# Performance work log

Measured on AMD Instinct MI355X. Metric: run time of the kernel, lower is better.

## Reference

```python
import jax, jax.numpy as jnp
import numpy as np
import math

D_MODEL = 1024
N_HEADS = 16
HEAD_DIM = D_MODEL // N_HEADS
MLP_DIM = 4 * D_MODEL
B, L, M = 2, 2048, 2048


def layer_norm(x, g, b, eps=1e-5):
    mu = jnp.mean(x, axis=-1, keepdims=True)
    var = jnp.var(x, axis=-1, keepdims=True)
    return (x - mu) * jax.lax.rsqrt(var + eps) * g + b


def mha(q_in, k_in, qW, wW, oW, mask=None):
    # Faithful to source: k and v share w_proj, and the value einsum uses k.
    b, l, _ = q_in.shape
    m = k_in.shape[1]
    q = (q_in @ qW).reshape(b, l, HEAD_DIM, N_HEADS)
    k = (k_in @ wW).reshape(b, m, HEAD_DIM, N_HEADS)
    s = jnp.einsum('bldn,bmdn->blmn', q, k)
    if mask is not None:
        s = jnp.where(mask, -1e9, s)  # mask applied BEFORE scaling, as in source
    s = s / math.sqrt(HEAD_DIM)
    w = jax.nn.softmax(s, axis=2)
    x = jnp.einsum('blmn,bmdn->bldn', w, k)  # source bug: uses k, not v
    x = x.reshape(b, l, HEAD_DIM * N_HEADS)
    return x @ oW


def setup_inputs() -> dict:
    key = jax.random.key(0)
    ks = jax.random.split(key, 16)
    sc = 1.0 / math.sqrt(D_MODEL)
    inp = {
        'x': jax.random.normal(ks[0], (B, L, D_MODEL), jnp.float32),
        'enc_output': jax.random.normal(ks[1], (B, M, D_MODEL), jnp.float32),
        'mask': jax.random.randint(ks[2], (B, 1, M, 1), 0, 2).astype(bool),
        'q1W': jax.random.normal(ks[3], (D_MODEL, D_MODEL), jnp.float32) * sc,
        'w1W': jax.random.normal(ks[4], (D_MODEL, D_MODEL), jnp.float32) * sc,
        'o1W': jax.random.normal(ks[5], (D_MODEL, D_MODEL), jnp.float32) * sc,
        'q2W': jax.random.normal(ks[6], (D_MODEL, D_MODEL), jnp.float32) * sc,
        'w2W': jax.random.normal(ks[7], (D_MODEL, D_MODEL), jnp.float32) * sc,
        'o2W': jax.random.normal(ks[8], (D_MODEL, D_MODEL), jnp.float32) * sc,
        'ffW1': jax.random.normal(ks[9], (D_MODEL, MLP_DIM), jnp.float32) * sc,
        'ffb1': jnp.zeros((MLP_DIM,), jnp.float32),
        'ffW2': jax.random.normal(ks[10], (MLP_DIM, D_MODEL), jnp.float32) * sc,
        'ffb2': jnp.zeros((D_MODEL,), jnp.float32),
        'g1': jnp.ones((D_MODEL,), jnp.float32), 'b1': jnp.zeros((D_MODEL,), jnp.float32),
        'g2': jnp.ones((D_MODEL,), jnp.float32), 'b2': jnp.zeros((D_MODEL,), jnp.float32),
        'g3': jnp.ones((D_MODEL,), jnp.float32), 'b3': jnp.zeros((D_MODEL,), jnp.float32),
    }
    return inp


def reference(x, enc_output, mask, q1W, w1W, o1W, q2W, w2W, o2W,
              ffW1, ffb1, ffW2, ffb2, g1, b1, g2, b2, g3, b3):
    # self-attention (no mask, as in source)
    sa = mha(x, x, q1W, w1W, o1W, mask=None)
    x = layer_norm(x + sa, g1, b1)
    # encoder-decoder attention with mask
    ca = mha(x, enc_output, q2W, w2W, o2W, mask=mask)
    x = layer_norm(x + ca, g2, b2)
    # feed-forward (exact GELU, matching torch nn.GELU default)
    h = jax.nn.gelu(x @ ffW1 + ffb1, approximate=False)
    ff = h @ ffW2 + ffb2
    x = layer_norm(x + ff, g3, b3)
    return x
```

## Files before the change

kernel.cpp:

```cpp
#include <hip/hip_runtime.h>
#include <hip/hip_bf16.h>
#include <math.h>
#include <stdint.h>

typedef __attribute__((ext_vector_type(8))) short bf16x8_t;
typedef __attribute__((ext_vector_type(4))) float f32x4_t;

#define LOG2E 1.4426950408889634f
#define GLB(p) ((const __attribute__((address_space(1))) void*)(p))
#define LDS(p) ((__attribute__((address_space(3))) void*)(p))

__device__ __forceinline__ unsigned short f2bf(float f) {
    union { float f; unsigned int u; } v; v.f = f;
    unsigned int r = v.u + 0x7FFFu + ((v.u >> 16) & 1u);
    return (unsigned short)(r >> 16);
}

__device__ __forceinline__ float bf2f(unsigned short us) {
    union { unsigned int u; float f; } c; c.u = (unsigned int)us << 16; return c.f;
}

__device__ __forceinline__ unsigned int pack2bf(float a, float b) {
#if __has_builtin(__builtin_amdgcn_cvt_pk_bf16_f32)
    auto r = __builtin_amdgcn_cvt_pk_bf16_f32(a, b);
    unsigned int u;
    __builtin_memcpy(&u, &r, 4);
    return u;
#else
    return (unsigned int)f2bf(a) | ((unsigned int)f2bf(b) << 16);
#endif
}

__device__ __forceinline__ float fast_rcp(float x) {
#if __has_builtin(__builtin_amdgcn_rcpf)
    return __builtin_amdgcn_rcpf(x);
#else
    return 1.0f / x;
#endif
}

__device__ __forceinline__ float gelu_fast(float v) {
    float x2 = v * v;
    float inner = v * fmaf(0.0356774081f, x2, 0.7978845608f);
    inner = fminf(fmaxf(inner, -20.f), 20.f);
    float t = exp2f(inner * 2.8853900817779268f);
    return v * t * fast_rcp(t + 1.0f);
}

__global__ void cast2_bf16_k(const float* __restrict__ inA, unsigned short* __restrict__ outA,
                             const float* __restrict__ inB, unsigned short* __restrict__ outB,
                             int n4, const int* __restrict__ maskp, float* __restrict__ mask4) {
    if (blockIdx.y == 2) {
        int i = blockIdx.x * blockDim.x + threadIdx.x;
        if (i < 8192) {
            int nt = i & 3, l16 = (i >> 2) & 15, t = (i >> 6) & 31, b = (i >> 11) & 1;
            mask4[i] = maskp[b * 2048 + t * 64 + nt * 16 + l16] ? -1e10f : 0.0f;
        }
        return;
    }
    const float* in = blockIdx.y ? inB : inA;
    unsigned short* out = blockIdx.y ? outB : outA;
    int i = blockIdx.x * blockDim.x + threadIdx.x;
    if (i < n4) {
        float4 v = ((const float4*)in)[i];
        ushort4 o;
        o.x = f2bf(v.x); o.y = f2bf(v.y); o.z = f2bf(v.z); o.w = f2bf(v.w);
        ((ushort4*)out)[i] = o;
    }
}

__global__ void transpose_all_k(const float* __restrict__ s0, const float* __restrict__ s1,
                                const float* __restrict__ s2, const float* __restrict__ s3,
                                const float* __restrict__ s4, const float* __restrict__ s5,
                                const float* __restrict__ s6, const float* __restrict__ s7,
                                unsigned short* __restrict__ d0, unsigned short* __restrict__ d1,
                                unsigned short* __restrict__ d2, unsigned short* __restrict__ d3,
                                unsigned short* __restrict__ d4, unsigned short* __restrict__ d5,
                                unsigned short* __restrict__ d6, unsigned short* __restrict__ d7) {
    __shared__ float tile[32][33];
    int idx = blockIdx.x;
    const float* W; unsigned short* Wt; int K, N, bx, by;
    if (idx < 6144) {
        int which = idx >> 10, t = idx & 1023;
        bx = t & 31; by = t >> 5; K = 1024; N = 1024;
        switch (which) {
            case 0: W = s0; Wt = d0; break;
            case 1: W = s1; Wt = d1; break;
            case 2: W = s2; Wt = d2; break;
            case 3: W = s3; Wt = d3; break;
            case 4: W = s4; Wt = d4; break;
            default: W = s5; Wt = d5; break;
        }
    } else if (idx < 10240) {
        int t = idx - 6144;
        bx = t & 127; by = t >> 7; K = 1024; N = 4096;
        W = s6; Wt = d6;
    } else {
        int t = idx - 10240;
        bx = t & 31; by = t >> 5; K = 4096; N = 1024;
        W = s7; Wt = d7;
    }
    int k0 = by * 32, n0 = bx * 32;
    int tx = threadIdx.x, ty = threadIdx.y;
#pragma unroll
    for (int i = 0; i < 32; i += 8)
        tile[ty + i][tx] = W[(long)(k0 + ty + i) * N + n0 + tx];
    __syncthreads();
#pragma unroll
    for (int i = 0; i < 32; i += 8)
        Wt[(long)(n0 + ty + i) * K + k0 + tx] = f2bf(tile[tx][ty + i]);
}

__global__ __launch_bounds__(256) void split_qk_k(const unsigned short* __restrict__ inQ,
                                                  const unsigned short* __restrict__ inK,
                                                  int stride, int koff,
                                                  unsigned short* __restrict__ Qout,
                                                  unsigned short* __restrict__ Kout) {
    __shared__ __align__(16) unsigned short t[16][1024];
    long l0 = (long)blockIdx.x * 16;
    int tid = threadIdx.x;
    int h = tid >> 4, lr = tid & 15;
    long l = l0 + lr;
    int b = (int)(l >> 11);
    int ll = (int)(l & 2047);
    int sw = ll & 7;

    for (int c = tid; c < 2048; c += 256) {
        int r = c >> 7, col = (c & 127) * 8;
        *(uint4*)(&t[r][col]) = *(const uint4*)(inQ + (l0 + r) * stride + col);
    }
    __syncthreads();
    {
        unsigned short* op = Qout + ((long)(b * 16 + h) * 2048 + ll) * 64;
#pragma unroll
        for (int g = 0; g < 8; g++) {
            union { uint4 v; unsigned short s[8]; } u;
#pragma unroll
            for (int j = 0; j < 8; j++) u.s[j] = t[lr][(g * 8 + j) * 16 + h];
            *(uint4*)(op + (g ^ sw) * 8) = u.v;
        }
    }
    __syncthreads();
    for (int c = tid; c < 2048; c += 256) {
        int r = c >> 7, col = (c & 127) * 8;
        *(uint4*)(&t[r][col]) = *(const uint4*)(inK + (l0 + r) * stride + koff + col);
    }
    __syncthreads();
    {
        unsigned short* op = Kout + ((long)(b * 16 + h) * 2048 + ll) * 64;
#pragma unroll
        for (int g = 0; g < 8; g++) {
            union { uint4 v; unsigned short s[8]; } u;
#pragma unroll
            for (int j = 0; j < 8; j++) u.s[j] = t[lr][(g * 8 + j) * 16 + h];
            *(uint4*)(op + (g ^ sw) * 8) = u.v;
        }
    }
}

__global__ __launch_bounds__(256) void transpose_heads_perm_k(const unsigned short* __restrict__ in,
                                                              unsigned short* __restrict__ out) {
    __shared__ unsigned short t[64][72];
    int bh = blockIdx.y;
    int m0 = blockIdx.x * 64;
    int tid = threadIdx.x;
    for (int c = tid; c < 512; c += 256) {
        int r = c >> 3, gp = c & 7;
        int glog = gp ^ (r & 7);
        uint4 v = *(const uint4*)(in + ((long)bh * 2048 + m0 + r) * 64 + gp * 8);
        *(uint4*)(&t[r][glog * 8]) = v;
    }
    __syncthreads();
    for (int c = tid; c < 512; c += 256) {
        int d = c >> 3, pb = (c & 7) * 8;
        union { uint4 v; unsigned short s[8]; } u;
#pragma unroll
        for (int j = 0; j < 8; j++) {
            int p = pb + j;
            int m = (p >> 2) + (p & 3) * 16;
            u.s[j] = t[m][d];
        }
        int gph = (pb >> 3) ^ (d & 7);
        *(uint4*)(out + ((long)bh * 64 + d) * 2048 + m0 + gph * 8) = u.v;
    }
}

template <int EP, int BN>
__global__ __launch_bounds__(256) void gemm_k(const unsigned short* __restrict__ A,
                                              const unsigned short* __restrict__ Bt,
                                              void* __restrict__ outp,
                                              const float* __restrict__ bias,
                                              int M, int N, int K) {
    __shared__ __align__(16) unsigned short As[128 * 64];
    __shared__ __align__(16) unsigned short Bs[BN * 64];
    const int NT = BN / 32;
    const int BG = BN / 32;
    int tid = threadIdx.x;
    int wave = tid >> 6, lane = tid & 63;
    int wm = wave >> 1, wn = wave & 1;
    int quad = lane >> 4, l16 = lane & 15;
    int bm = blockIdx.y * 128, bn = blockIdx.x * BN;

    f32x4_t acc[4][NT] = {};

    int srow = tid >> 3;
    int sgrp = (tid & 7) ^ (srow & 7);
    const unsigned short* Ag[4];
#pragma unroll
    for (int i = 0; i < 4; i++)
        Ag[i] = A + (long)(bm + i * 32 + srow) * K + sgrp * 8;
    const unsigned short* Bg[BG];
#pragma unroll
    for (int i = 0; i < BG; i++)
        Bg[i] = Bt + (long)(bn + i * 32 + srow) * K + sgrp * 8;

    for (int k0 = 0; k0 < K; k0 += 64) {
        __syncthreads();
#pragma unroll
        for (int i = 0; i < 4; i++)
            __builtin_amdgcn_global_load_lds(GLB(Ag[i] + k0), LDS(As + i * 2048 + tid * 8), 16, 0, 0);
#pragma unroll
        for (int i = 0; i < BG; i++)
            __builtin_amdgcn_global_load_lds(GLB(Bg[i] + k0), LDS(Bs + i * 2048 + tid * 8), 16, 0, 0);
        __syncthreads();
#pragma unroll
        for (int kk = 0; kk < 2; kk++) {
            int xg = ((kk * 4 + quad) ^ (l16 & 7)) * 8;
            bf16x8_t af[4], bfr[NT];
#pragma unroll
            for (int t = 0; t < 4; t++)
                af[t] = *(const bf16x8_t*)(As + (wm * 64 + t * 16 + l16) * 64 + xg);
#pragma unroll
            for (int t = 0; t < NT; t++)
                bfr[t] = *(const bf16x8_t*)(Bs + (wn * (BN / 2) + t * 16 + l16) * 64 + xg);
#pragma unroll
            for (int mt = 0; mt < 4; mt++)
#pragma unroll
                for (int nt = 0; nt < NT; nt++)
                    acc[mt][nt] = __builtin_amdgcn_mfma_f32_16x16x32_bf16(af[mt], bfr[nt], acc[mt][nt], 0, 0, 0);
        }
    }

#pragma unroll
    for (int mt = 0; mt < 4; mt++)
#pragma unroll
        for (int nt = 0; nt < NT; nt++)
#pragma unroll
            for (int r = 0; r < 4; r++) {
                int gm = bm + wm * 64 + mt * 16 + quad * 4 + r;
                int gn = bn + wn * (BN / 2) + nt * 16 + l16;
                float v = acc[mt][nt][r];
                if (EP == 0) {
                    ((float*)outp)[(long)gm * N + gn] = v;
                } else if (EP == 2) {
                    v = gelu_fast(v + bias[gn]);
                    ((unsigned short*)outp)[(long)gm * N + gn] = f2bf(v);
                } else if (EP == 3) {
                    ((float*)outp)[(long)gm * N + gn] = v + bias[gn];
                } else if (EP == 6) {
                    ((unsigned short*)outp)[(long)gm * N + gn] = f2bf(v + bias[gn]);
                } else {
                    ((unsigned short*)outp)[(long)gm * N + gn] = f2bf(v);
                }
            }
}

template <int EP>
__global__ __launch_bounds__(512, 4) void gemm8_k(const unsigned short* __restrict__ A,
                                                  const unsigned short* __restrict__ Bt,
                                                  void* __restrict__ outp,
                                                  const float* __restrict__ bias,
                                                  const unsigned short* __restrict__ A2,
                                                  const unsigned short* __restrict__ Bt2,
                                                  void* __restrict__ out2,
                                                  int M, int N, int K) {
    if (blockIdx.z) { A = A2; Bt = Bt2; outp = out2; }
    __shared__ __align__(16) unsigned short As[2 * 128 * 64];
    __shared__ __align__(16) unsigned short Bs[2 * 128 * 64];
    int tid = threadIdx.x;
    int wave = tid >> 6, lane = tid & 63;
    int wm = wave >> 2, wn = wave & 3;
    int quad = lane >> 4, l16 = lane & 15;
    int bm = blockIdx.y * 128, bn = blockIdx.x * 128;

    f32x4_t acc[4][2] = {};

    int srow = tid >> 3;
    int sgrp = (tid & 7) ^ (srow & 7);
    const unsigned short* Ag[2];
    const unsigned short* Bg[2];
#pragma unroll
    for (int i = 0; i < 2; i++) {
        Ag[i] = A + (long)(bm + i * 64 + srow) * K + sgrp * 8;
        Bg[i] = Bt + (long)(bn + i * 64 + srow) * K + sgrp * 8;
    }

    auto stage = [&](int buf, int k0) {
#pragma unroll
        for (int i = 0; i < 2; i++)
            __builtin_amdgcn_global_load_lds(GLB(Ag[i] + k0), LDS(As + buf * 8192 + i * 4096 + tid * 8), 16, 0, 0);
#pragma unroll
        for (int i = 0; i < 2; i++)
            __builtin_amdgcn_global_load_lds(GLB(Bg[i] + k0), LDS(Bs + buf * 8192 + i * 4096 + tid * 8), 16, 0, 0);
    };

    auto compute = [&](int buf) {
        const unsigned short* Ab = As + buf * 8192;
        const unsigned short* Bb = Bs + buf * 8192;
#pragma unroll
        for (int kk = 0; kk < 2; kk++) {
            int xg = ((kk * 4 + quad) ^ (l16 & 7)) * 8;
            bf16x8_t af[4], bfr[2];
#pragma unroll
            for (int t = 0; t < 4; t++)
                af[t] = *(const bf16x8_t*)(Ab + (wm * 64 + t * 16 + l16) * 64 + xg);
#pragma unroll
            for (int t = 0; t < 2; t++)
                bfr[t] = *(const bf16x8_t*)(Bb + (wn * 32 + t * 16 + l16) * 64 + xg);
#pragma unroll
            for (int mt = 0; mt < 4; mt++)
#pragma unroll
                for (int nt = 0; nt < 2; nt++)
                    acc[mt][nt] = __builtin_amdgcn_mfma_f32_16x16x32_bf16(af[mt], bfr[nt], acc[mt][nt], 0, 0, 0);
        }
    };

    stage(0, 0);
    const int NS = K >> 6;
    for (int i = 0; i < NS; i++) {
        if (i + 1 < NS) {
            stage((i + 1) & 1, (i + 1) << 6);
            asm volatile("s_waitcnt vmcnt(4)\n\ts_barrier" ::: "memory");
        } else {
            asm volatile("s_waitcnt vmcnt(0)\n\ts_barrier" ::: "memory");
        }
        compute(i & 1);
        asm volatile("s_barrier" ::: "memory");
    }

#pragma unroll
    for (int mt = 0; mt < 4; mt++)
#pragma unroll
        for (int nt = 0; nt < 2; nt++)
#pragma unroll
            for (int r = 0; r < 4; r++) {
                int gm = bm + wm * 64 + mt * 16 + quad * 4 + r;
                int gn = bn + wn * 32 + nt * 16 + l16;
                float v = acc[mt][nt][r];
                if (EP == 6) {
                    ((unsigned short*)outp)[(long)gm * N + gn] = f2bf(v + bias[gn]);
                } else {
                    ((unsigned short*)outp)[(long)gm * N + gn] = f2bf(v);
                }
            }
}

template <int USE_MASK>
__global__ __launch_bounds__(256, 4) void flash_attn9_k(const unsigned short* __restrict__ Qh,
                                                        const unsigned short* __restrict__ Kh,
                                                        const unsigned short* __restrict__ KhTp,
                                                        const float* __restrict__ mask4,
                                                        unsigned short* __restrict__ out) {
    __shared__ __align__(16) unsigned short K1[64 * 64];
    __shared__ __align__(16) unsigned short K2[64 * 64];
    __shared__ __align__(16) unsigned short Ps[64 * 64];
    __shared__ __align__(16) float Ml[USE_MASK ? 2048 : 4];

    int tid = threadIdx.x;
    int wave = tid >> 6, lane = tid & 63;
    int quad = lane >> 4, l16 = lane & 15;
    int bh = blockIdx.y, b = bh >> 4, h = bh & 15;
    int l0 = blockIdx.x * 64;
    const unsigned short* k1p = Kh + (long)bh * 2048 * 64 + tid * 8;
    const unsigned short* k2p = KhTp + (long)bh * 64 * 2048 + (long)(tid >> 3) * 2048 + (tid & 7) * 8;

    int sw = l16 & 7;

    const unsigned short* qrow = Qh + ((long)bh * 2048 + l0 + wave * 16 + l16) * 64;
    bf16x8_t qf[2];
#pragma unroll
    for (int kk = 0; kk < 2; kk++)
        qf[kk] = *(const bf16x8_t*)(qrow + ((kk * 4 + quad) ^ sw) * 8);

    __builtin_amdgcn_global_load_lds(GLB(k1p), LDS(K1 + tid * 8), 16, 0, 0);
    __builtin_amdgcn_global_load_lds(GLB(k1p + 2048), LDS(K1 + tid * 8 + 2048), 16, 0, 0);
    __builtin_amdgcn_global_load_lds(GLB(k2p), LDS(K2 + tid * 8), 16, 0, 0);
    __builtin_amdgcn_global_load_lds(GLB(k2p + 32 * 2048), LDS(K2 + tid * 8 + 2048), 16, 0, 0);
    if (USE_MASK) {
        const float* mp = mask4 + b * 2048;
        for (int c = tid; c < 512; c += 256)
            ((float4*)Ml)[c] = ((const float4*)mp)[c];
    }
    __syncthreads();

    const float C1 = 0.125f * LOG2E;
    f32x4_t acc_o[4] = {};
    float rs[4] = {0.f, 0.f, 0.f, 0.f};

    for (int t = 0; t < 32; ++t) {
        uint4 rA, rB, rC, rD;
        if (t < 31) {
            k1p += 4096;
            k2p += 64;
            rA = *(const uint4*)(k1p);
            rB = *(const uint4*)(k1p + 2048);
            rC = *(const uint4*)(k2p);
            rD = *(const uint4*)(k2p + 32 * 2048);
        }

        float4 mq = make_float4(0.f, 0.f, 0.f, 0.f);
        if (USE_MASK) mq = *(const float4*)(Ml + t * 64 + l16 * 4);

        f32x4_t sacc[4] = {};
        __builtin_amdgcn_s_setprio(1);
#pragma unroll
        for (int kk = 0; kk < 2; kk++) {
            int xg = ((kk * 4 + quad) ^ sw) * 8;
#pragma unroll
            for (int nt = 0; nt < 4; nt++) {
                bf16x8_t bfr = *(const bf16x8_t*)(K1 + (nt * 16 + l16) * 64 + xg);
                sacc[nt] = __builtin_amdgcn_mfma_f32_16x16x32_bf16(qf[kk], bfr, sacc[nt], 0, 0, 0);
            }
        }
        __builtin_amdgcn_s_setprio(0);

#pragma unroll
        for (int r = 0; r < 4; r++) {
            float p0 = exp2f(fmaf(sacc[0][r], C1, mq.x));
            float p1 = exp2f(fmaf(sacc[1][r], C1, mq.y));
            float p2 = exp2f(fmaf(sacc[2][r], C1, mq.z));
            float p3 = exp2f(fmaf(sacc[3][r], C1, mq.w));
            rs[r] += (p0 + p1) + (p2 + p3);
            uint2 pk; pk.x = pack2bf(p0, p1); pk.y = pack2bf(p2, p3);
            int Rrow = wave * 16 + quad * 4 + r;
            int grp = (l16 >> 1) ^ (Rrow & 7);
            *(uint2*)(Ps + Rrow * 64 + grp * 8 + (l16 & 1) * 4) = pk;
        }

        __builtin_amdgcn_s_setprio(1);
#pragma unroll
        for (int kk = 0; kk < 2; kk++) {
            int xg = ((kk * 4 + quad) ^ sw) * 8;
            int Rr = wave * 16 + l16;
            int pg = ((kk * 4 + quad) ^ (l16 & 7)) * 8;
            bf16x8_t af = *(const bf16x8_t*)(Ps + Rr * 64 + pg);
#pragma unroll
            for (int nt = 0; nt < 4; nt++) {
                bf16x8_t bfr = *(const bf16x8_t*)(K2 + (nt * 16 + l16) * 64 + xg);
                acc_o[nt] = __builtin_amdgcn_mfma_f32_16x16x32_bf16(af, bfr, acc_o[nt], 0, 0, 0);
            }
        }
        __builtin_amdgcn_s_setprio(0);

        asm volatile("s_barrier" ::: "memory");
        if (t < 31) {
            *(uint4*)(K1 + tid * 8) = rA;
            *(uint4*)(K1 + tid * 8 + 2048) = rB;
            *(uint4*)(K2 + tid * 8) = rC;
            *(uint4*)(K2 + tid * 8 + 2048) = rD;
            asm volatile("s_waitcnt lgkmcnt(0)\n\ts_barrier" ::: "memory");
        }
    }

#pragma unroll
    for (int r = 0; r < 4; r++) {
#pragma unroll
        for (int d = 1; d < 16; d <<= 1) rs[r] += __shfl_xor(rs[r], d);
    }

#pragma unroll
    for (int r = 0; r < 4; r++) {
        float inv = 1.0f / rs[r];
        int l = l0 + wave * 16 + quad * 4 + r;
#pragma unroll
        for (int nt = 0; nt < 4; nt++) {
            int d = nt * 16 + l16;
            out[((long)(b * 2048 + l)) * 1024 + d * 16 + h] = f2bf(acc_o[nt][r] * inv);
        }
    }
}

template <int AIN_BF16, int OUT_F32>
__global__ __launch_bounds__(256) void resid_ln_k(const void* __restrict__ ap,
                                                  const unsigned short* __restrict__ rb,
                                                  const float* __restrict__ g,
                                                  const float* __restrict__ bb,
                                                  float* __restrict__ outf,
                                                  unsigned short* __restrict__ outb) {
    long row = blockIdx.x;
    int tid = threadIdx.x;
    float x0, x1, x2, x3;
    if (AIN_BF16) {
        ushort4 va = ((const ushort4*)((const unsigned short*)ap + row * 1024))[tid];
        x0 = bf2f(va.x); x1 = bf2f(va.y); x2 = bf2f(va.z); x3 = bf2f(va.w);
    } else {
        float4 va = ((const float4*)((const float*)ap + row * 1024))[tid];
        x0 = va.x; x1 = va.y; x2 = va.z; x3 = va.w;
    }
    ushort4 vr = ((const ushort4*)(rb + row * 1024))[tid];
    x0 += bf2f(vr.x); x1 += bf2f(vr.y); x2 += bf2f(vr.z); x3 += bf2f(vr.w);
    float s = x0 + x1 + x2 + x3;
    float sq = x0 * x0 + x1 * x1 + x2 * x2 + x3 * x3;
#pragma unroll
    for (int d = 1; d < 64; d <<= 1) { s += __shfl_xor(s, d); sq += __shfl_xor(sq, d); }
    __shared__ float ss[4], ssq[4];
    int wave = tid >> 6, lane = tid & 63;
    if (lane == 0) { ss[wave] = s; ssq[wave] = sq; }
    __syncthreads();
    s = ss[0] + ss[1] + ss[2] + ss[3];
    sq = ssq[0] + ssq[1] + ssq[2] + ssq[3];
    float mean = s * (1.0f / 1024.0f);
    float var = sq * (1.0f / 1024.0f) - mean * mean;
    float rstd = rsqrtf(var + 1e-5f);
    float4 vg = ((const float4*)g)[tid];
    float4 vb = ((const float4*)bb)[tid];
    float y0 = (x0 - mean) * rstd * vg.x + vb.x;
    float y1 = (x1 - mean) * rstd * vg.y + vb.y;
    float y2 = (x2 - mean) * rstd * vg.z + vb.z;
    float y3 = (x3 - mean) * rstd * vg.w + vb.w;
    if (OUT_F32) {
        float4 o; o.x = y0; o.y = y1; o.z = y2; o.w = y3;
        ((float4*)(outf + row * 1024))[tid] = o;
    } else {
        ushort4 ob; ob.x = f2bf(y0); ob.y = f2bf(y1); ob.z = f2bf(y2); ob.w = f2bf(y3);
        ((ushort4*)(outb + row * 1024))[tid] = ob;
    }
}

extern "C" void kernel_launch(void* const* d_in, const int* in_sizes, int n_in,
                              void* d_out, int out_size, void* d_ws, size_t ws_size,
                              hipStream_t stream) {
    const float* x    = (const float*)d_in[0];
    const float* enc  = (const float*)d_in[1];
    const int*   mask = (const int*)d_in[2];
    const float* q1W  = (const float*)d_in[3];
    const float* w1W  = (const float*)d_in[4];
    const float* o1W  = (const float*)d_in[5];
    const float* q2W  = (const float*)d_in[6];
    const float* w2W  = (const float*)d_in[7];
    const float* o2W  = (const float*)d_in[8];
    const float* ffW1 = (const float*)d_in[9];
    const float* ffb1 = (const float*)d_in[10];
    const float* ffW2 = (const float*)d_in[11];
    const float* ffb2 = (const float*)d_in[12];
    const float* g1 = (const float*)d_in[13];
    const float* b1 = (const float*)d_in[14];
    const float* g2 = (const float*)d_in[15];
    const float* b2 = (const float*)d_in[16];
    const float* g3 = (const float*)d_in[17];
    const float* b3 = (const float*)d_in[18];
    float* outp = (float*)d_out;

    const int T = 4096;
    const int D = 1024;
    const int F = 4096;

    char* ws = (char*)d_ws;
    auto alloc = [&](size_t sz) { char* p = ws; ws += (sz + 255) & ~(size_t)255; return p; };
    unsigned short* qw1Wt = (unsigned short*)alloc((size_t)2 * D * D * 2);
    unsigned short* o1Wt  = (unsigned short*)alloc((size_t)D * D * 2);
    unsigned short* q2Wt  = (unsigned short*)alloc((size_t)D * D * 2);
    unsigned short* w2Wt  = (unsigned short*)alloc((size_t)D * D * 2);
    unsigned short* o2Wt  = (unsigned short*)alloc((size_t)D * D * 2);
    unsigned short* ffW1t = (unsigned short*)alloc((size_t)F * D * 2);
    unsigned short* ffW2t = (unsigned short*)alloc((size_t)D * F * 2);
    unsigned short* xb    = (unsigned short*)alloc((size_t)T * D * 2);
    unsigned short* encb  = (unsigned short*)alloc((size_t)T * D * 2);
    unsigned short* Qhb   = (unsigned short*)alloc((size_t)T * D * 2);
    unsigned short* Khb   = (unsigned short*)alloc((size_t)T * D * 2);
    unsigned short* KhTb  = (unsigned short*)alloc((size_t)T * D * 2);
    unsigned short* attnb = (unsigned short*)alloc((size_t)T * D * 2);
    float*          mask4b= (float*)alloc((size_t)8192 * 4);
    unsigned short* projb = (unsigned short*)alloc((size_t)T * D * 2);
    unsigned short* x1s   = (unsigned short*)alloc((size_t)T * D * 2);
    unsigned short* x2s   = (unsigned short*)alloc((size_t)T * D * 2);
    unsigned short* S1    = (unsigned short*)alloc((size_t)T * F * 2);
    unsigned short* tmpqw = S1;
    unsigned short* q2o   = S1;
    unsigned short* w2o   = S1 + (size_t)T * D;
    unsigned short* hb    = S1;

    dim3 blk256(256);
    dim3 blk512(512);
    dim3 tblk(32, 8);

    cast2_bf16_k<<<dim3(T * D / 4 / 256, 3), blk256, 0, stream>>>(x, xb, enc, encb, T * D / 4, mask, mask4b);
    transpose_all_k<<<dim3(14336), tblk, 0, stream>>>(
        q1W, w1W, o1W, q2W, w2W, o2W, ffW1, ffW2,
        qw1Wt, qw1Wt + (size_t)D * D, o1Wt, q2Wt, w2Wt, o2Wt, ffW1t, ffW2t);

    gemm8_k<4><<<dim3(2 * D / 128, T / 128, 1), blk512, 0, stream>>>(
        xb, qw1Wt, tmpqw, nullptr, nullptr, nullptr, nullptr, T, 2 * D, D);
    split_qk_k<<<dim3(T / 16), blk256, 0, stream>>>(tmpqw, tmpqw, 2 * D, D, Qhb, Khb);
    transpose_heads_perm_k<<<dim3(32, 32), blk256, 0, stream>>>(Khb, KhTb);
    flash_attn9_k<0><<<dim3(32, 32), blk256, 0, stream>>>(Qhb, Khb, KhTb, nullptr, attnb);
    gemm8_k<4><<<dim3(D / 128, T / 128, 1), blk512, 0, stream>>>(
        attnb, o1Wt, projb, nullptr, nullptr, nullptr, nullptr, T, D, D);
    resid_ln_k<0, 0><<<dim3(T), blk256, 0, stream>>>(x, projb, g1, b1, nullptr, x1s);

    gemm8_k<4><<<dim3(D / 128, T / 128, 2), blk512, 0, stream>>>(
        x1s, q2Wt, q2o, nullptr, encb, w2Wt, w2o, T, D, D);
    split_qk_k<<<dim3(T / 16), blk256, 0, stream>>>(q2o, w2o, D, 0, Qhb, Khb);
    transpose_heads_perm_k<<<dim3(32, 32), blk256, 0, stream>>>(Khb, KhTb);
    flash_attn9_k<1><<<dim3(32, 32), blk256, 0, stream>>>(Qhb, Khb, KhTb, mask4b, attnb);
    gemm8_k<4><<<dim3(D / 128, T / 128, 1), blk512, 0, stream>>>(
        attnb, o2Wt, projb, nullptr, nullptr, nullptr, nullptr, T, D, D);
    resid_ln_k<1, 0><<<dim3(T), blk256, 0, stream>>>(x1s, projb, g2, b2, nullptr, x2s);

    gemm_k<2, 128><<<dim3(F / 128, T / 128, 1), blk256, 0, stream>>>(
        x2s, ffW1t, hb, ffb1, T, F, D);
    gemm8_k<6><<<dim3(D / 128, T / 128, 1), blk512, 0, stream>>>(
        hb, ffW2t, projb, ffb2, nullptr, nullptr, nullptr, T, D, F);
    resid_ln_k<1, 1><<<dim3(T), blk256, 0, stream>>>(x2s, projb, g3, b3, outp, nullptr);
}
```

Before: 560.8 us.

## Fuse head split and K transpose into Q/K projection GEMM epilogue

The Q/K projection GEMMs now stage their bf16 output tile in shared memory and write Q, K and the permuted transposed K straight into head-major swizzled layouts. This removes the separate split_qk and transpose_heads kernels along with the round trip through an intermediate buffer. Exp2 calls in the attention softmax and GELU are also switched to the hardware exp2 intrinsic. In exchange, the GEMM epilogue gains extra LDS traffic, a block-wide sync and less coalesced scattered stores.

```diff
diff --git a/kernel.cpp b/kernel.cpp
--- a/kernel.cpp
+++ b/kernel.cpp
@@ -39,11 +39,19 @@
 #endif
 }
 
+__device__ __forceinline__ float fexp2(float x) {
+#if __has_builtin(__builtin_amdgcn_exp2f)
+    return __builtin_amdgcn_exp2f(x);
+#else
+    return exp2f(x);
+#endif
+}
+
 __device__ __forceinline__ float gelu_fast(float v) {
     float x2 = v * v;
     float inner = v * fmaf(0.0356774081f, x2, 0.7978845608f);
     inner = fminf(fmaxf(inner, -20.f), 20.f);
-    float t = exp2f(inner * 2.8853900817779268f);
+    float t = fexp2(inner * 2.8853900817779268f);
     return v * t * fast_rcp(t + 1.0f);
 }
 
@@ -111,80 +119,6 @@
         Wt[(long)(n0 + ty + i) * K + k0 + tx] = f2bf(tile[tx][ty + i]);
 }
 
-__global__ __launch_bounds__(256) void split_qk_k(const unsigned short* __restrict__ inQ,
-                                                  const unsigned short* __restrict__ inK,
-                                                  int stride, int koff,
-                                                  unsigned short* __restrict__ Qout,
-                                                  unsigned short* __restrict__ Kout) {
-    __shared__ __align__(16) unsigned short t[16][1024];
-    long l0 = (long)blockIdx.x * 16;
-    int tid = threadIdx.x;
-    int h = tid >> 4, lr = tid & 15;
-    long l = l0 + lr;
-    int b = (int)(l >> 11);
-    int ll = (int)(l & 2047);
-    int sw = ll & 7;
-
-    for (int c = tid; c < 2048; c += 256) {
-        int r = c >> 7, col = (c & 127) * 8;
-        *(uint4*)(&t[r][col]) = *(const uint4*)(inQ + (l0 + r) * stride + col);
-    }
-    __syncthreads();
-    {
-        unsigned short* op = Qout + ((long)(b * 16 + h) * 2048 + ll) * 64;
-#pragma unroll
-        for (int g = 0; g < 8; g++) {
-            union { uint4 v; unsigned short s[8]; } u;
-#pragma unroll
-            for (int j = 0; j < 8; j++) u.s[j] = t[lr][(g * 8 + j) * 16 + h];
-            *(uint4*)(op + (g ^ sw) * 8) = u.v;
-        }
-    }
-    __syncthreads();
-    for (int c = tid; c < 2048; c += 256) {
-        int r = c >> 7, col = (c & 127) * 8;
-        *(uint4*)(&t[r][col]) = *(const uint4*)(inK + (l0 + r) * stride + koff + col);
-    }
-    __syncthreads();
-    {
-        unsigned short* op = Kout + ((long)(b * 16 + h) * 2048 + ll) * 64;
-#pragma unroll
-        for (int g = 0; g < 8; g++) {
-            union { uint4 v; unsigned short s[8]; } u;
-#pragma unroll
-            for (int j = 0; j < 8; j++) u.s[j] = t[lr][(g * 8 + j) * 16 + h];
-            *(uint4*)(op + (g ^ sw) * 8) = u.v;
-        }
-    }
-}
-
-__global__ __launch_bounds__(256) void transpose_heads_perm_k(const unsigned short* __restrict__ in,
-                                                              unsigned short* __restrict__ out) {
-    __shared__ unsigned short t[64][72];
-    int bh = blockIdx.y;
-    int m0 = blockIdx.x * 64;
-    int tid = threadIdx.x;
-    for (int c = tid; c < 512; c += 256) {
-        int r = c >> 3, gp = c & 7;
-        int glog = gp ^ (r & 7);
-        uint4 v = *(const uint4*)(in + ((long)bh * 2048 + m0 + r) * 64 + gp * 8);
-        *(uint4*)(&t[r][glog * 8]) = v;
-    }
-    __syncthreads();
-    for (int c = tid; c < 512; c += 256) {
-        int d = c >> 3, pb = (c & 7) * 8;
-        union { uint4 v; unsigned short s[8]; } u;
-#pragma unroll
-        for (int j = 0; j < 8; j++) {
-            int p = pb + j;
-            int m = (p >> 2) + (p & 3) * 16;
-            u.s[j] = t[m][d];
-        }
-        int gph = (pb >> 3) ^ (d & 7);
-        *(uint4*)(out + ((long)bh * 64 + d) * 2048 + m0 + gph * 8) = u.v;
-    }
-}
-
 template <int EP, int BN>
 __global__ __launch_bounds__(256) void gemm_k(const unsigned short* __restrict__ A,
                                               const unsigned short* __restrict__ Bt,
@@ -250,15 +184,9 @@
                 int gm = bm + wm * 64 + mt * 16 + quad * 4 + r;
                 int gn = bn + wn * (BN / 2) + nt * 16 + l16;
                 float v = acc[mt][nt][r];
-                if (EP == 0) {
-                    ((float*)outp)[(long)gm * N + gn] = v;
-                } else if (EP == 2) {
+                if (EP == 2) {
                     v = gelu_fast(v + bias[gn]);
                     ((unsigned short*)outp)[(long)gm * N + gn] = f2bf(v);
-                } else if (EP == 3) {
-                    ((float*)outp)[(long)gm * N + gn] = v + bias[gn];
-                } else if (EP == 6) {
-                    ((unsigned short*)outp)[(long)gm * N + gn] = f2bf(v + bias[gn]);
                 } else {
                     ((unsigned short*)outp)[(long)gm * N + gn] = f2bf(v);
                 }
@@ -272,11 +200,14 @@
                                                   const float* __restrict__ bias,
                                                   const unsigned short* __restrict__ A2,
                                                   const unsigned short* __restrict__ Bt2,
-                                                  void* __restrict__ out2,
+                                                  unsigned short* __restrict__ qout,
+                                                  unsigned short* __restrict__ kout,
+                                                  unsigned short* __restrict__ ktout,
                                                   int M, int N, int K) {
-    if (blockIdx.z) { A = A2; Bt = Bt2; outp = out2; }
-    __shared__ __align__(16) unsigned short As[2 * 128 * 64];
-    __shared__ __align__(16) unsigned short Bs[2 * 128 * 64];
+    if (blockIdx.z) { A = A2; Bt = Bt2; }
+    __shared__ __align__(16) unsigned short SMEM[32768];
+    unsigned short* As = SMEM;
+    unsigned short* Bs = SMEM + 16384;
     int tid = threadIdx.x;
     int wave = tid >> 6, lane = tid & 63;
     int wm = wave >> 2, wn = wave & 3;
@@ -336,6 +267,64 @@
         }
         compute(i & 1);
         asm volatile("s_barrier" ::: "memory");
+    }
+
+    if (EP == 7 || EP == 8) {
+        bool kmode = (EP == 7) ? (bn >= 1024) : (blockIdx.z != 0);
+        int G = (EP == 7 && kmode) ? ((bn - 1024) >> 7) : (bn >> 7);
+        unsigned short* Ct = SMEM;
+#pragma unroll
+        for (int mt = 0; mt < 4; mt++)
+#pragma unroll
+            for (int nt = 0; nt < 2; nt++)
+#pragma unroll
+                for (int r = 0; r < 4; r++) {
+                    int rr = wm * 64 + mt * 16 + quad * 4 + r;
+                    int cc = wn * 32 + nt * 16 + l16;
+                    Ct[rr * 132 + cc] = f2bf(acc[mt][nt][r]);
+                }
+        __syncthreads();
+        int bq = bm >> 11;
+        if (!kmode) {
+#pragma unroll
+            for (int i = 0; i < 4; i++) {
+                int e = tid + i * 512;
+                int h = e & 15, rl = e >> 4;
+                int ll = (bm & 2047) + rl;
+                union { uint4 v; unsigned short s[8]; } u;
+#pragma unroll
+                for (int j = 0; j < 8; j++) u.s[j] = Ct[rl * 132 + j * 16 + h];
+                *(uint4*)(qout + (((long)(bq * 16 + h) * 2048 + ll) << 6) + ((G ^ (ll & 7)) << 3)) = u.v;
+            }
+        } else {
+#pragma unroll
+            for (int i = 0; i < 4; i++) {
+                int e = tid + i * 512;
+                int h = e & 15, rl = e >> 4;
+                int mm = (bm & 2047) + rl;
+                union { uint4 v; unsigned short s[8]; } u;
+#pragma unroll
+                for (int j = 0; j < 8; j++) u.s[j] = Ct[rl * 132 + j * 16 + h];
+                *(uint4*)(kout + (((long)(bq * 16 + h) * 2048 + mm) << 6) + ((G ^ (mm & 7)) << 3)) = u.v;
+            }
+#pragma unroll
+            for (int i = 0; i < 4; i++) {
+                int e = tid + i * 512;
+                int glog = e & 7, m0s = (e >> 3) & 1, dl = (e >> 4) & 7, h = e >> 7;
+                int d = G * 8 + dl;
+                union { uint4 v; unsigned short s[8]; } u;
+#pragma unroll
+                for (int j = 0; j < 8; j++) {
+                    int p = glog * 8 + j;
+                    int ml = (p >> 2) + (p & 3) * 16;
+                    u.s[j] = Ct[(m0s * 64 + ml) * 132 + dl * 16 + h];
+                }
+                int mmbase = (bm & 2047) + m0s * 64;
+                int gph = glog ^ (d & 7);
+                *(uint4*)(ktout + ((long)(bq * 16 + h) * 64 + d) * 2048 + mmbase + gph * 8) = u.v;
+            }
+        }
+        return;
     }
 
 #pragma unroll
@@ -426,10 +415,10 @@
 
 #pragma unroll
         for (int r = 0; r < 4; r++) {
-            float p0 = exp2f(fmaf(sacc[0][r], C1, mq.x));
-            float p1 = exp2f(fmaf(sacc[1][r], C1, mq.y));
-            float p2 = exp2f(fmaf(sacc[2][r], C1, mq.z));
-            float p3 = exp2f(fmaf(sacc[3][r], C1, mq.w));
+            float p0 = fexp2(fmaf(sacc[0][r], C1, mq.x));
+            float p1 = fexp2(fmaf(sacc[1][r], C1, mq.y));
+            float p2 = fexp2(fmaf(sacc[2][r], C1, mq.z));
+            float p3 = fexp2(fmaf(sacc[3][r], C1, mq.w));
             rs[r] += (p0 + p1) + (p2 + p3);
             uint2 pk; pk.x = pack2bf(p0, p1); pk.y = pack2bf(p2, p3);
             int Rrow = wave * 16 + quad * 4 + r;
@@ -575,9 +564,6 @@
     unsigned short* x1s   = (unsigned short*)alloc((size_t)T * D * 2);
     unsigned short* x2s   = (unsigned short*)alloc((size_t)T * D * 2);
     unsigned short* S1    = (unsigned short*)alloc((size_t)T * F * 2);
-    unsigned short* tmpqw = S1;
-    unsigned short* q2o   = S1;
-    unsigned short* w2o   = S1 + (size_t)T * D;
     unsigned short* hb    = S1;
 
     dim3 blk256(256);
@@ -589,27 +575,23 @@
         q1W, w1W, o1W, q2W, w2W, o2W, ffW1, ffW2,
         qw1Wt, qw1Wt + (size_t)D * D, o1Wt, q2Wt, w2Wt, o2Wt, ffW1t, ffW2t);
 
-    gemm8_k<4><<<dim3(2 * D / 128, T / 128, 1), blk512, 0, stream>>>(
-        xb, qw1Wt, tmpqw, nullptr, nullptr, nullptr, nullptr, T, 2 * D, D);
-    split_qk_k<<<dim3(T / 16), blk256, 0, stream>>>(tmpqw, tmpqw, 2 * D, D, Qhb, Khb);
-    transpose_heads_perm_k<<<dim3(32, 32), blk256, 0, stream>>>(Khb, KhTb);
+    gemm8_k<7><<<dim3(2 * D / 128, T / 128, 1), blk512, 0, stream>>>(
+        xb, qw1Wt, nullptr, nullptr, nullptr, nullptr, Qhb, Khb, KhTb, T, 2 * D, D);
     flash_attn9_k<0><<<dim3(32, 32), blk256, 0, stream>>>(Qhb, Khb, KhTb, nullptr, attnb);
     gemm8_k<4><<<dim3(D / 128, T / 128, 1), blk512, 0, stream>>>(
-        attnb, o1Wt, projb, nullptr, nullptr, nullptr, nullptr, T, D, D);
+        attnb, o1Wt, projb, nullptr, nullptr, nullptr, nullptr, nullptr, nullptr, T, D, D);
     resid_ln_k<0, 0><<<dim3(T), blk256, 0, stream>>>(x, projb, g1, b1, nullptr, x1s);
 
-    gemm8_k<4><<<dim3(D / 128, T / 128, 2), blk512, 0, stream>>>(
-        x1s, q2Wt, q2o, nullptr, encb, w2Wt, w2o, T, D, D);
-    split_qk_k<<<dim3(T / 16), blk256, 0, stream>>>(q2o, w2o, D, 0, Qhb, Khb);
-    transpose_heads_perm_k<<<dim3(32, 32), blk256, 0, stream>>>(Khb, KhTb);
+    gemm8_k<8><<<dim3(D / 128, T / 128, 2), blk512, 0, stream>>>(
+        x1s, q2Wt, nullptr, nullptr, encb, w2Wt, Qhb, Khb, KhTb, T, D, D);
     flash_attn9_k<1><<<dim3(32, 32), blk256, 0, stream>>>(Qhb, Khb, KhTb, mask4b, attnb);
     gemm8_k<4><<<dim3(D / 128, T / 128, 1), blk512, 0, stream>>>(
-        attnb, o2Wt, projb, nullptr, nullptr, nullptr, nullptr, T, D, D);
+        attnb, o2Wt, projb, nullptr, nullptr, nullptr, nullptr, nullptr, nullptr, T, D, D);
     resid_ln_k<1, 0><<<dim3(T), blk256, 0, stream>>>(x1s, projb, g2, b2, nullptr, x2s);
 
     gemm_k<2, 128><<<dim3(F / 128, T / 128, 1), blk256, 0, stream>>>(
         x2s, ffW1t, hb, ffb1, T, F, D);
     gemm8_k<6><<<dim3(D / 128, T / 128, 1), blk512, 0, stream>>>(
-        hb, ffW2t, projb, ffb2, nullptr, nullptr, nullptr, T, D, F);
+        hb, ffW2t, projb, ffb2, nullptr, nullptr, nullptr, nullptr, nullptr, T, D, F);
     resid_ln_k<1, 1><<<dim3(T), blk256, 0, stream>>>(x2s, projb, g3, b3, outp, nullptr);
 }
```

Result: faster. 490.7 us (-12.5%).
